# Performance work log

Measured on AMD Instinct MI355X. Metric: run time of the kernel, lower is better.

The kernel has to match this reference:

```python
import jax, jax.numpy as jnp
import numpy as np

N_NODES = 20000
N_EDGES = 320000
F_IN = 64
F = 64            # n_features
K = 32            # n_basis_funcs
R = 3             # n_refinements
R_MAX = 2.5       # radial basis span


def setup_inputs() -> dict:
    key = jax.random.key(0)
    ks = jax.random.split(key, 16)
    inp = {
        "x_dftb": jax.random.normal(ks[0], (N_NODES, 4, F_IN), jnp.float32),
        "coords": jax.random.normal(ks[1], (N_NODES, 3), jnp.float32),
        "dst_idx": jax.random.randint(ks[2], (N_EDGES,), 0, N_NODES, jnp.int32),
        "src_idx": jax.random.randint(ks[3], (N_EDGES,), 0, N_NODES, jnp.int32),
        # input TensorDense (degree-wise dense; bias only on the l=0 channel)
        "W_in0": jax.random.normal(ks[4], (F_IN, F), jnp.float32) / np.sqrt(F_IN),
        "W_in1": jax.random.normal(ks[5], (F_IN, F), jnp.float32) / np.sqrt(F_IN),
        "b_in": jnp.zeros((F,), jnp.float32),
        # per-refinement MessagePass params: basis projection (K->F) + scalar-channel bias
        "W_basis": jax.random.normal(ks[6], (R, K, F), jnp.float32) / np.sqrt(K),
        "b_basis": jnp.zeros((R, F), jnp.float32),
        # per-refinement CG path weights: 5 paths (0x0->0, 1.1->0, 0x1->1, 1x0->1, 1x1->1)
        "path_w": 0.05 * jax.random.normal(ks[7], (R, 5, F), jnp.float32),
        # output TensorDense (F -> 1)
        "W_out0": jax.random.normal(ks[8], (F, 1), jnp.float32) / np.sqrt(F),
        "W_out1": jax.random.normal(ks[9], (F, 1), jnp.float32) / np.sqrt(F),
        "b_out": jnp.zeros((1,), jnp.float32),
    }
    return inp


def _tensor_dense(x, W0, W1, b0):
    # degree-wise dense mixing of channels; bias only on l=0 (keeps equivariance)
    s = jnp.einsum('nf,fg->ng', x[:, 0], W0) + b0          # (N, G)
    v = jnp.einsum('nif,fg->nig', x[:, 1:4], W1)           # (N, 3, G)
    return jnp.concatenate([s[:, None], v], axis=1)        # (N, 4, G)


def reference(x_dftb, coords, dst_idx, src_idx,
              W_in0, W_in1, b_in, W_basis, b_basis, path_w,
              W_out0, W_out1, b_out):
    N = x_dftb.shape[0]
    # edge geometry: dist basis = gaussian radial x spherical harmonics (l<=1)
    r = coords[dst_idx] - coords[src_idx]                  # (E, 3)
    d = jnp.sqrt(jnp.sum(r * r, axis=-1) + 1e-12)          # (E,)
    rhat = r / d[:, None]
    sh = jnp.concatenate([jnp.ones_like(d)[:, None], rhat], axis=1)  # (E, 4)
    centers = jnp.linspace(0.0, R_MAX, K, dtype=jnp.float32)
    width = centers[1] - centers[0]
    rbf = jnp.exp(-((d[:, None] - centers) / width) ** 2)  # (E, K)
    basis = sh[:, :, None] * rbf[:, None, :]               # (E, 4, K)

    x = _tensor_dense(x_dftb, W_in0, W_in1, b_in)          # (N, 4, F)
    n_ref = W_basis.shape[0]
    for i in range(n_ref):
        # project basis channels K -> F, bias on scalar channel (use_basis_bias)
        g = jnp.einsum('elk,kf->elf', basis, W_basis[i])   # (E, 4, F)
        g = g.at[:, 0, :].add(b_basis[i])
        a = x[src_idx]                                     # gather src  (E, 4, F)
        a0, av = a[:, 0], a[:, 1:4]
        g0, gv = g[:, 0], g[:, 1:4]
        p = path_w[i]
        # CG-structured tensor product per feature channel
        m0 = p[0] * a0 * g0 + p[1] * jnp.sum(av * gv, axis=1)                 # (E, F)
        mv = (p[2][None, None] * a0[:, None] * gv
              + p[3][None, None] * av * g0[:, None]
              + p[4][None, None] * jnp.cross(av, gv, axis=1))                 # (E, 3, F)
        msg = jnp.concatenate([m0[:, None], mv], axis=1)                      # (E, 4, F)
        x = x + jax.ops.segment_sum(msg, dst_idx, num_segments=N)            # scatter-add
    return _tensor_dense(x, W_out0, W_out1, b_out)         # (N, 4, 1)
```

## Files before the change

### kernel.cpp

```cpp
#include <hip/hip_runtime.h>

#define N_NODES 20000
#define N_EDGES 320000
#define FF 64
#define KK 32
#define EPAD 460032
#define GT 64
#define BW 8

typedef _Float16 half4v __attribute__((ext_vector_type(4)));
typedef short bf16x8 __attribute__((ext_vector_type(8)));
typedef float fx4 __attribute__((ext_vector_type(4)));

__device__ __forceinline__ unsigned short f2bf(float x) {
    unsigned u = __float_as_uint(x);
    unsigned r = (u + 0x7FFFu + ((u >> 16) & 1u)) >> 16;
    return (unsigned short)r;
}

__global__ __launch_bounds__(256) void hist_k(const int* __restrict__ dst,
                                              int* __restrict__ cnt) {
    int e = blockIdx.x * 256 + threadIdx.x;
    if (e >= N_EDGES) return;
    atomicAdd(&cnt[dst[e]], 1);
}

__global__ __launch_bounds__(1024) void scan_k(const int* __restrict__ cnt,
                                               int* __restrict__ rps) {
    __shared__ int part[1024];
    int t = threadIdx.x;
    const int CH = 20;
    int lo = t * CH;
    int hi = lo + CH; if (hi > N_NODES) hi = N_NODES;
    int s = 0;
    for (int i = lo; i < hi && lo < N_NODES; ++i) s += (cnt[i] + 7) & ~7;
    if (lo >= N_NODES) s = 0;
    part[t] = s;
    __syncthreads();
    for (int off = 1; off < 1024; off <<= 1) {
        int tmp = (t >= off) ? part[t - off] : 0;
        __syncthreads();
        part[t] += tmp;
        __syncthreads();
    }
    int excl = part[t] - s;
    if (lo < N_NODES) {
        int run = excl;
        for (int i = lo; i < hi; ++i) { rps[i] = run; run += (cnt[i] + 7) & ~7; }
    }
    if (t == 1023) rps[N_NODES] = part[1023];
}

__global__ __launch_bounds__(256) void scatter_k(const float* __restrict__ coords,
                                                 const int* __restrict__ dst,
                                                 const int* __restrict__ src,
                                                 const int* __restrict__ rps,
                                                 int* __restrict__ fill,
                                                 int* __restrict__ esrcB,
                                                 float4* __restrict__ egeom) {
    int e = blockIdx.x * 256 + threadIdx.x;
    if (e >= N_EDGES) return;
    int di = dst[e], si = src[e];
    int pos = rps[di] + atomicAdd(&fill[di], 1);
    float rx = coords[di*3+0] - coords[si*3+0];
    float ry = coords[di*3+1] - coords[si*3+1];
    float rz = coords[di*3+2] - coords[si*3+2];
    float d = sqrtf(rx*rx + ry*ry + rz*rz + 1e-12f);
    float inv = 1.0f / d;
    esrcB[pos] = si * 512;
    egeom[pos] = make_float4(d, rx*inv, ry*inv, rz*inv);
}

__global__ __launch_bounds__(256) void pad_k(const int* __restrict__ rps,
                                             const int* __restrict__ cnt,
                                             int* __restrict__ esrcB,
                                             float4* __restrict__ egeom) {
    int n = blockIdx.x * 256 + threadIdx.x;
    if (n >= N_NODES) return;
    int fin = rps[n] + cnt[n];
    int stop = rps[n+1];
    for (int e = fin; e < stop; ++e) {
        esrcB[e] = N_NODES * 512;
        egeom[e] = make_float4(1.f, 0.f, 0.f, 0.f);
    }
}

template<int NR>
__global__ __launch_bounds__(256) void gmatM_k(const float4* __restrict__ egeom,
                                               const float* __restrict__ Wb,
                                               const int* __restrict__ rps,
                                               half4v* __restrict__ G4) {
    __shared__ __align__(16) short WtL[NR*KK*FF];
    __shared__ __align__(16) short rbfL[2][GT*40];
    int t = threadIdx.x;
    for (int idx = t; idx < NR*KK*FF; idx += 256)
        WtL[idx] = (short)f2bf(Wb[idx]);
    __syncthreads();

    int lane = t & 63, q = t >> 6;
    int kb = lane >> 4, cl = lane & 15;

    bf16x8 Bfr[NR][4];
    #pragma unroll
    for (int r = 0; r < NR; ++r) {
        #pragma unroll
        for (int nb = 0; nb < 4; ++nb) {
            bf16x8 fr;
            #pragma unroll
            for (int e2 = 0; e2 < 8; ++e2)
                fr[e2] = WtL[r*2048 + (kb*8 + e2)*64 + nb*16 + cl];
            Bfr[r][nb] = fr;
        }
    }

    int total = rps[N_NODES];
    int ntiles = (total + GT - 1) / GT;
    const float inv_w = 31.0f / 2.5f;
    int buf = 0;
    for (int tile = blockIdx.x; tile < ntiles; tile += gridDim.x) {
        int e0 = tile * GT;
        {
            int ew = t & 63;
            float d = egeom[e0 + ew].x;
            float t0 = d * inv_w;
            int k0 = (int)floorf(t0 + 0.5f) - 4;
            if (k0 < 0) k0 = 0;
            if (k0 > KK - 9) k0 = KK - 9;
            bf16x8 pk;
            #pragma unroll
            for (int i2 = 0; i2 < 8; ++i2) {
                int j = q*8 + i2;
                float dt = t0 - (float)j;
                float v = (j >= k0 && j < k0 + 9) ? __expf(-dt * dt) : 0.f;
                pk[i2] = (short)f2bf(v);
            }
            *(bf16x8*)(&rbfL[buf][ew*40 + q*8]) = pk;
        }
        __syncthreads();
        bf16x8 afr = *(const bf16x8*)(&rbfL[buf][(q*16 + cl)*40 + kb*8]);
        int eg = (e0 + q*16 + kb*4) >> 2;
        #pragma unroll
        for (int r = 0; r < NR; ++r) {
            #pragma unroll
            for (int nb = 0; nb < 4; ++nb) {
                fx4 dacc = {0.f, 0.f, 0.f, 0.f};
                dacc = __builtin_amdgcn_mfma_f32_16x16x32_bf16(afr, Bfr[r][nb],
                                                               dacc, 0, 0, 0);
                half4v hv;
                hv[0] = (_Float16)dacc[0]; hv[1] = (_Float16)dacc[1];
                hv[2] = (_Float16)dacc[2]; hv[3] = (_Float16)dacc[3];
                G4[(size_t)r*(EPAD/4)*64 + (size_t)eg*64 + nb*16 + cl] = hv;
            }
        }
        buf ^= 1;
    }
}

__global__ __launch_bounds__(256) void node_inM_k(const float* __restrict__ x_dftb,
                                                  const float* __restrict__ W0,
                                                  const float* __restrict__ W1,
                                                  const float* __restrict__ bin,
                                                  float* __restrict__ x,
                                                  half4v* __restrict__ xh) {
    int t = threadIdx.x;
    int q = t >> 6, lane = t & 63;
    int kb = lane >> 4, cl = lane & 15;
    int w = blockIdx.x * 4 + q;
    if (w >= N_NODES / 16) return;
    int n0 = w * 16;

    bf16x8 BF[2][4][2];
    #pragma unroll
    for (int cb = 0; cb < 4; ++cb) {
        #pragma unroll
        for (int kf = 0; kf < 2; ++kf) {
            bf16x8 f0, f1;
            #pragma unroll
            for (int j = 0; j < 8; ++j) {
                int k = kf*32 + kb*8 + j;
                f0[j] = (short)f2bf(W0[k*64 + cb*16 + cl]);
                f1[j] = (short)f2bf(W1[k*64 + cb*16 + cl]);
            }
            BF[0][cb][kf] = f0;
            BF[1][cb][kf] = f1;
        }
    }
    float bb[4];
    #pragma unroll
    for (int cb = 0; cb < 4; ++cb) bb[cb] = bin[cb*16 + cl];

    fx4 acc[4][4];
    #pragma unroll
    for (int l = 0; l < 4; ++l) {
        const float* xr = x_dftb + (size_t)(n0 + cl)*256 + l*64 + kb*8;
        float4 v0 = *(const float4*)(xr);
        float4 v1 = *(const float4*)(xr + 4);
        float4 v2 = *(const float4*)(xr + 32);
        float4 v3 = *(const float4*)(xr + 36);
        bf16x8 a0, a1;
        a0[0]=(short)f2bf(v0.x); a0[1]=(short)f2bf(v0.y);
        a0[2]=(short)f2bf(v0.z); a0[3]=(short)f2bf(v0.w);
        a0[4]=(short)f2bf(v1.x); a0[5]=(short)f2bf(v1.y);
        a0[6]=(short)f2bf(v1.z); a0[7]=(short)f2bf(v1.w);
        a1[0]=(short)f2bf(v2.x); a1[1]=(short)f2bf(v2.y);
        a1[2]=(short)f2bf(v2.z); a1[3]=(short)f2bf(v2.w);
        a1[4]=(short)f2bf(v3.x); a1[5]=(short)f2bf(v3.y);
        a1[6]=(short)f2bf(v3.z); a1[7]=(short)f2bf(v3.w);
        const int wsel = (l == 0) ? 0 : 1;
        #pragma unroll
        for (int cb = 0; cb < 4; ++cb) {
            fx4 c = {0.f, 0.f, 0.f, 0.f};
            c = __builtin_amdgcn_mfma_f32_16x16x32_bf16(a0, BF[wsel][cb][0], c, 0, 0, 0);
            c = __builtin_amdgcn_mfma_f32_16x16x32_bf16(a1, BF[wsel][cb][1], c, 0, 0, 0);
            acc[l][cb] = c;
        }
    }

    #pragma unroll
    for (int cb = 0; cb < 4; ++cb) {
        int f = cb*16 + cl;
        #pragma unroll
        for (int reg = 0; reg < 4; ++reg) {
            int n = n0 + kb*4 + reg;
            float a0v = acc[0][cb][reg] + bb[cb];
            float a1v = acc[1][cb][reg];
            float a2v = acc[2][cb][reg];
            float a3v = acc[3][cb][reg];
            *(float4*)(x + (size_t)n*256 + f*4) = make_float4(a0v, a1v, a2v, a3v);
            half4v hs;
            hs[0] = (_Float16)a0v; hs[1] = (_Float16)a1v;
            hs[2] = (_Float16)a2v; hs[3] = (_Float16)a3v;
            xh[(size_t)n*64 + f] = hs;
        }
    }
}

__global__ __launch_bounds__(256) void node_in_k(const float* __restrict__ x_dftb,
                                                 const float* __restrict__ W0,
                                                 const float* __restrict__ W1,
                                                 const float* __restrict__ bin,
                                                 float* __restrict__ x,
                                                 half4v* __restrict__ xh) {
    int t = threadIdx.x;
    int q = t >> 6, f = t & 63;
    int n = blockIdx.x * 4 + q;
    float w0r[64], w1r[64];
    #pragma unroll
    for (int k = 0; k < 64; ++k) { w0r[k] = W0[k*64 + f]; w1r[k] = W1[k*64 + f]; }
    float a0 = bin[f], a1 = 0.f, a2 = 0.f, a3 = 0.f;
    const float4* xr = (const float4*)(x_dftb + (size_t)n * 256);
    #pragma unroll
    for (int j = 0; j < 16; ++j) {
        float4 x0 = xr[j];
        float4 x1 = xr[16 + j];
        float4 x2 = xr[32 + j];
        float4 x3 = xr[48 + j];
        a0 += x0.x*w0r[4*j] + x0.y*w0r[4*j+1] + x0.z*w0r[4*j+2] + x0.w*w0r[4*j+3];
        a1 += x1.x*w1r[4*j] + x1.y*w1r[4*j+1] + x1.z*w1r[4*j+2] + x1.w*w1r[4*j+3];
        a2 += x2.x*w1r[4*j] + x2.y*w1r[4*j+1] + x2.z*w1r[4*j+2] + x2.w*w1r[4*j+3];
        a3 += x3.x*w1r[4*j] + x3.y*w1r[4*j+1] + x3.z*w1r[4*j+2] + x3.w*w1r[4*j+3];
    }
    *(float4*)(x + (size_t)n*256 + f*4) = make_float4(a0, a1, a2, a3);
    if (xh) {
        half4v hs;
        hs[0] = (_Float16)a0; hs[1] = (_Float16)a1;
        hs[2] = (_Float16)a2; hs[3] = (_Float16)a3;
        xh[(size_t)n*64 + f] = hs;
    }
}

template<int LAST>
__global__ __launch_bounds__(256) void msg_fast_k(const int* __restrict__ rps,
                                                  const int* __restrict__ esrcB,
                                                  const float4* __restrict__ egeom,
                                                  const half4v* __restrict__ G4,
                                                  const float* __restrict__ bbv,
                                                  const float* __restrict__ pw,
                                                  const float* __restrict__ xo_f,
                                                  const half4v* __restrict__ xo_h,
                                                  float* __restrict__ xn_f,
                                                  half4v* __restrict__ xn_h,
                                                  const float* __restrict__ Wo0,
                                                  const float* __restrict__ Wo1,
                                                  const float* __restrict__ bo,
                                                  float* __restrict__ out) {
    int t = threadIdx.x;
    int q = t >> 6, f = t & 63;

    float b_f = bbv[f];
    float p0 = pw[f], p1 = pw[64+f], p2 = pw[128+f], p3 = pw[192+f], p4 = pw[256+f];
    float w0 = 0.f, w1 = 0.f;
    if (LAST) { w0 = Wo0[f]; w1 = Wo1[f]; }

    const char* xob = (const char*)xo_h;
    int fb = f * 8;

    for (int n = blockIdx.x * 4 + q; n < N_NODES; n += gridDim.x * 4) {
        float4 self = *(const float4*)(xo_f + (size_t)n*256 + f*4);
        float acc0 = self.x, acc1 = self.y, acc2 = self.z, acc3 = self.w;

        int beg = rps[n], end = rps[n+1];
        for (int e0 = beg; e0 < end; e0 += BW) {
            int4 oa = *(const int4*)(esrcB + e0);
            int4 ob = *(const int4*)(esrcB + e0 + 4);
            int off[BW] = {oa.x, oa.y, oa.z, oa.w, ob.x, ob.y, ob.z, ob.w};
            half4v h[BW];
            #pragma unroll
            for (int j = 0; j < BW; ++j)
                h[j] = *(const half4v*)(xob + (size_t)(unsigned)off[j] + fb);
            half4v ga = G4[(size_t)(e0 >> 2)*64 + f];
            half4v gb = G4[(size_t)((e0 >> 2) + 1)*64 + f];
            float Gv[BW] = {(float)ga[0], (float)ga[1], (float)ga[2], (float)ga[3],
                            (float)gb[0], (float)gb[1], (float)gb[2], (float)gb[3]};
            float4 g4[BW];
            #pragma unroll
            for (int j = 0; j < BW; ++j) g4[j] = egeom[e0 + j];

            #pragma unroll
            for (int j = 0; j < BW; ++j) {
                float A0 = (float)h[j][0], A1 = (float)h[j][1];
                float A2 = (float)h[j][2], A3 = (float)h[j][3];
                float G = Gv[j];
                float ry = g4[j].y, rz = g4[j].z, rw_ = g4[j].w;
                float g0v = G + b_f;
                float dotav = A1*ry + A2*rz + A3*rw_;
                acc0 += p0*A0*g0v + p1*dotav*G;
                float tA = p2*A0*G, tB = p3*g0v, tC = p4*G;
                acc1 += tA*ry  + tB*A1 + tC*(A2*rw_ - A3*rz);
                acc2 += tA*rz  + tB*A2 + tC*(A3*ry  - A1*rw_);
                acc3 += tA*rw_ + tB*A3 + tC*(A1*rz  - A2*ry);
            }
        }

        if (LAST) {
            float s0 = acc0 * w0, s1 = acc1 * w1, s2 = acc2 * w1, s3 = acc3 * w1;
            #pragma unroll
            for (int off2 = 32; off2 >= 1; off2 >>= 1) {
                s0 += __shfl_down(s0, off2, 64);
                s1 += __shfl_down(s1, off2, 64);
                s2 += __shfl_down(s2, off2, 64);
                s3 += __shfl_down(s3, off2, 64);
            }
            if (f == 0) {
                float b = bo[0];
                out[n*4 + 0] = s0 + b;
                out[n*4 + 1] = s1;
                out[n*4 + 2] = s2;
                out[n*4 + 3] = s3;
            }
        } else {
            *(float4*)(xn_f + (size_t)n*256 + f*4) = make_float4(acc0, acc1, acc2, acc3);
            half4v hs;
            hs[0] = (_Float16)acc0; hs[1] = (_Float16)acc1;
            hs[2] = (_Float16)acc2; hs[3] = (_Float16)acc3;
            xn_h[(size_t)n*64 + f] = hs;
        }
    }
}

__global__ __launch_bounds__(256) void msg_slow_k(const int* __restrict__ rps,
                                                  const int* __restrict__ cnt,
                                                  const int* __restrict__ esrcB,
                                                  const float4* __restrict__ egeom,
                                                  const float* __restrict__ Wb,
                                                  const float* __restrict__ bbv,
                                                  const float* __restrict__ pw,
                                                  const float* __restrict__ xo_f,
                                                  float* __restrict__ xn_f) {
    int t = threadIdx.x;
    int n = blockIdx.x * 4 + (t >> 6);
    int f = t & 63;
    float wreg[KK];
    #pragma unroll
    for (int k = 0; k < KK; ++k) wreg[k] = Wb[k*64 + f];
    float4 self = *(const float4*)(xo_f + (size_t)n*256 + f*4);
    float acc0 = self.x, acc1 = self.y, acc2 = self.z, acc3 = self.w;
    float b_f = bbv[f];
    float p0 = pw[f], p1 = pw[64+f], p2 = pw[128+f], p3 = pw[192+f], p4 = pw[256+f];
    const float wdt = 2.5f / 31.0f, inv_w = 31.0f / 2.5f;
    float ck = wdt * (float)(f & 31);
    int beg = rps[n], end = beg + cnt[n];
    const char* xob = (const char*)xo_f;
    for (int e = beg; e < end; ++e) {
        int off = esrcB[e];
        float4 g4 = egeom[e];
        float4 v = *(const float4*)(xob + ((size_t)(unsigned)off << 1) + f*16);
        float tt = (g4.x - ck) * inv_w;
        float my_rbf = __expf(-tt * tt);
        float Gs = 0.f;
        #pragma unroll
        for (int k = 0; k < KK; ++k) Gs += __shfl(my_rbf, k, 64) * wreg[k];
        float g0v = Gs + b_f;
        float dotav = v.y*g4.y + v.z*g4.z + v.w*g4.w;
        acc0 += p0*v.x*g0v + p1*dotav*Gs;
        float tA = p2*v.x*Gs, tB = p3*g0v, tC = p4*Gs;
        acc1 += tA*g4.y + tB*v.y + tC*(v.z*g4.w - v.w*g4.z);
        acc2 += tA*g4.z + tB*v.z + tC*(v.w*g4.y - v.y*g4.w);
        acc3 += tA*g4.w + tB*v.w + tC*(v.y*g4.z - v.z*g4.y);
    }
    *(float4*)(xn_f + (size_t)n*256 + f*4) = make_float4(acc0, acc1, acc2, acc3);
}

__global__ __launch_bounds__(256) void node_out_k(const float* __restrict__ x,
                                                  const float* __restrict__ W0,
                                                  const float* __restrict__ W1,
                                                  const float* __restrict__ bout,
                                                  float* __restrict__ out) {
    int n = blockIdx.x * 4 + (threadIdx.x >> 6);
    int f = threadIdx.x & 63;
    float w0 = W0[f], w1 = W1[f];
    float4 v = *(const float4*)(x + (size_t)n*256 + f*4);
    float s0 = v.x * w0, s1 = v.y * w1, s2 = v.z * w1, s3 = v.w * w1;
    #pragma unroll
    for (int off = 32; off >= 1; off >>= 1) {
        s0 += __shfl_down(s0, off, 64);
        s1 += __shfl_down(s1, off, 64);
        s2 += __shfl_down(s2, off, 64);
        s3 += __shfl_down(s3, off, 64);
    }
    if (f == 0) {
        float b = bout[0];
        out[n*4 + 0] = s0 + b;
        out[n*4 + 1] = s1;
        out[n*4 + 2] = s2;
        out[n*4 + 3] = s3;
    }
}

extern "C" void kernel_launch(void* const* d_in, const int* in_sizes, int n_in,
                              void* d_out, int out_size, void* d_ws, size_t ws_size,
                              hipStream_t stream) {
    const float* x_dftb  = (const float*)d_in[0];
    const float* coords  = (const float*)d_in[1];
    const int*   dst     = (const int*)  d_in[2];
    const int*   src     = (const int*)  d_in[3];
    const float* W_in0   = (const float*)d_in[4];
    const float* W_in1   = (const float*)d_in[5];
    const float* b_in    = (const float*)d_in[6];
    const float* W_basis = (const float*)d_in[7];
    const float* b_basis = (const float*)d_in[8];
    const float* path_w  = (const float*)d_in[9];
    const float* W_out0  = (const float*)d_in[10];
    const float* W_out1  = (const float*)d_in[11];
    const float* b_out   = (const float*)d_in[12];
    float* out = (float*)d_out;

    const size_t XF = (size_t)N_NODES * 256 * 4;
    const size_t XH = (size_t)(N_NODES + 1) * 64 * 8;
    const size_t EG = (size_t)EPAD * 16;
    const size_t ES = (size_t)EPAD * 4;
    const size_t GP = (size_t)EPAD * 64 * 2;
    const size_t RP = (((size_t)(N_NODES + 1) * 4) + 15) & ~(size_t)15;
    const size_t CF = (size_t)N_NODES * 4;

    const size_t base_need = 2*XF + 2*XH + EG + ES + RP + 2*CF;
    int planes = (ws_size >= base_need + 3*GP) ? 3
               : (ws_size >= base_need + 1*GP) ? 1 : 0;

    char* p = (char*)d_ws;
    float*   xA = (float*)p;  p += XF;
    float*   xB = (float*)p;  p += XF;
    half4v*  hA = nullptr; half4v* hB = nullptr;
    half4v*  Gm = nullptr;
    if (planes) {
        hA = (half4v*)p;  p += XH;
        hB = (half4v*)p;  p += XH;
        Gm = (half4v*)p;  p += (size_t)planes * GP;
    }
    float4* egeom = (float4*)p;  p += EG;
    int*    esrcB = (int*)p;     p += ES;
    int*    rps   = (int*)p;     p += RP;
    int*    cnt   = (int*)p;     p += CF;
    int*    fill  = (int*)p;     p += CF;

    hipMemsetAsync(cnt,  0, CF, stream);
    hipMemsetAsync(fill, 0, CF, stream);
    if (planes) {
        hipMemsetAsync((char*)hA + (size_t)N_NODES*512, 0, 512, stream);
        hipMemsetAsync((char*)hB + (size_t)N_NODES*512, 0, 512, stream);
    }

    hist_k   <<<(N_EDGES+255)/256, 256, 0, stream>>>(dst, cnt);
    scan_k   <<<1, 1024, 0, stream>>>(cnt, rps);
    scatter_k<<<(N_EDGES+255)/256, 256, 0, stream>>>(coords, dst, src, rps, fill,
                                                     esrcB, egeom);
    pad_k    <<<(N_NODES+255)/256, 256, 0, stream>>>(rps, cnt, esrcB, egeom);
    if (planes)
        node_inM_k<<<(N_NODES/16 + 3)/4, 256, 0, stream>>>(x_dftb, W_in0, W_in1,
                                                           b_in, xA, hA);
    else
        node_in_k<<<N_NODES/4, 256, 0, stream>>>(x_dftb, W_in0, W_in1, b_in, xA,
                                                 nullptr);
    if (planes == 3)
        gmatM_k<3><<<1536, 256, 0, stream>>>(egeom, W_basis, rps, Gm);

    float*  xo = xA; float*  xn = xB;
    half4v* ho = hA; half4v* hn = hB;
    for (int i = 0; i < 3; ++i) {
        if (planes) {
            if (planes == 1)
                gmatM_k<1><<<1536, 256, 0, stream>>>(egeom, W_basis + i*KK*FF, rps, Gm);
            const half4v* Gp = Gm + ((planes == 3) ? (size_t)i*(EPAD/4)*64 : 0);
            if (i < 2)
                msg_fast_k<0><<<2048, 256, 0, stream>>>(rps, esrcB, egeom, Gp,
                                                        b_basis + i*FF, path_w + i*5*FF,
                                                        xo, ho, xn, hn,
                                                        nullptr, nullptr, nullptr, nullptr);
            else
                msg_fast_k<1><<<2048, 256, 0, stream>>>(rps, esrcB, egeom, Gp,
                                                        b_basis + i*FF, path_w + i*5*FF,
                                                        xo, ho, nullptr, nullptr,
                                                        W_out0, W_out1, b_out, out);
        } else {
            msg_slow_k<<<N_NODES/4, 256, 0, stream>>>(rps, cnt, esrcB, egeom,
                                                      W_basis + i*KK*FF,
                                                      b_basis + i*FF, path_w + i*5*FF,
                                                      xo, xn);
        }
        float*  tf = xo; xo = xn; xn = tf;
        half4v* th = ho; ho = hn; hn = th;
    }
    if (!planes)
        node_out_k<<<N_NODES/4, 256, 0, stream>>>(xo, W_out0, W_out1, b_out, out);
}
```

Before: 271.0 us.

## Use packed fp16 math in message kernel with fp16 geometry planes

Adds a kernel that converts the per-edge direction vectors into packed fp16 planes grouped in blocks of 8 edges. The message kernel then does its per-edge tensor-product math in packed half2 arithmetic, two edges per instruction, and accumulates into fp32 once per 8-edge block. The launch also changes from a grid-stride loop over 2048 blocks to one node per wavefront with N/4 blocks. The aim is to halve ALU work and cut geometry bandwidth, at the cost of fp16 rounding inside each 8-edge partial sum.

Result: faster. 232.7 us (-14.1%).

```diff
diff --git a/kernel.cpp b/kernel.cpp
--- a/kernel.cpp
+++ b/kernel.cpp
@@ -9,6 +9,7 @@
 #define BW 8
 
 typedef _Float16 half4v __attribute__((ext_vector_type(4)));
+typedef _Float16 h2 __attribute__((ext_vector_type(2)));
 typedef short bf16x8 __attribute__((ext_vector_type(8)));
 typedef float fx4 __attribute__((ext_vector_type(4)));
 
@@ -16,6 +17,12 @@
     unsigned u = __float_as_uint(x);
     unsigned r = (u + 0x7FFFu + ((u >> 16) & 1u)) >> 16;
     return (unsigned short)r;
+}
+__device__ __forceinline__ h2 u2h(unsigned u) {
+    union { unsigned u; h2 h; } c; c.u = u; return c.h;
+}
+__device__ __forceinline__ unsigned h2u(h2 h) {
+    union { h2 h; unsigned u; } c; c.h = h; return c.u;
 }
 
 __global__ __launch_bounds__(256) void hist_k(const int* __restrict__ dst,
@@ -82,6 +89,27 @@
     for (int e = fin; e < stop; ++e) {
         esrcB[e] = N_NODES * 512;
         egeom[e] = make_float4(1.f, 0.f, 0.f, 0.f);
+    }
+}
+
+__global__ __launch_bounds__(256) void geomh_k(const float4* __restrict__ egeom,
+                                               const int* __restrict__ rps,
+                                               unsigned* __restrict__ gH) {
+    int b = blockIdx.x * 256 + threadIdx.x;
+    int total = rps[N_NODES];
+    if (b * 8 >= total) return;
+    float4 g[8];
+    #pragma unroll
+    for (int j = 0; j < 8; ++j) g[j] = egeom[b*8 + j];
+    unsigned* o = gH + (size_t)b * 12;
+    #pragma unroll
+    for (int p = 0; p < 4; ++p) {
+        h2 y; y[0] = (_Float16)g[2*p].y; y[1] = (_Float16)g[2*p+1].y;
+        h2 z; z[0] = (_Float16)g[2*p].z; z[1] = (_Float16)g[2*p+1].z;
+        h2 w; w[0] = (_Float16)g[2*p].w; w[1] = (_Float16)g[2*p+1].w;
+        o[0*4 + p] = h2u(y);
+        o[1*4 + p] = h2u(z);
+        o[2*4 + p] = h2u(w);
     }
 }
 
@@ -270,91 +298,115 @@
 }
 
 template<int LAST>
-__global__ __launch_bounds__(256) void msg_fast_k(const int* __restrict__ rps,
-                                                  const int* __restrict__ esrcB,
-                                                  const float4* __restrict__ egeom,
-                                                  const half4v* __restrict__ G4,
-                                                  const float* __restrict__ bbv,
-                                                  const float* __restrict__ pw,
-                                                  const float* __restrict__ xo_f,
-                                                  const half4v* __restrict__ xo_h,
-                                                  float* __restrict__ xn_f,
-                                                  half4v* __restrict__ xn_h,
-                                                  const float* __restrict__ Wo0,
-                                                  const float* __restrict__ Wo1,
-                                                  const float* __restrict__ bo,
-                                                  float* __restrict__ out) {
+__global__ __launch_bounds__(256) void msg_pk_k(const int* __restrict__ rps,
+                                                const int* __restrict__ esrcB,
+                                                const unsigned* __restrict__ gH,
+                                                const half4v* __restrict__ G4,
+                                                const float* __restrict__ bbv,
+                                                const float* __restrict__ pw,
+                                                const float* __restrict__ xo_f,
+                                                const half4v* __restrict__ xo_h,
+                                                float* __restrict__ xn_f,
+                                                half4v* __restrict__ xn_h,
+                                                const float* __restrict__ Wo0,
+                                                const float* __restrict__ Wo1,
+                                                const float* __restrict__ bo,
+                                                float* __restrict__ out) {
     int t = threadIdx.x;
     int q = t >> 6, f = t & 63;
+    int n = blockIdx.x * 4 + q;
+
+    float4 self = *(const float4*)(xo_f + (size_t)n*256 + f*4);
+    float acc0 = self.x, acc1 = self.y, acc2 = self.z, acc3 = self.w;
 
     float b_f = bbv[f];
-    float p0 = pw[f], p1 = pw[64+f], p2 = pw[128+f], p3 = pw[192+f], p4 = pw[256+f];
-    float w0 = 0.f, w1 = 0.f;
-    if (LAST) { w0 = Wo0[f]; w1 = Wo1[f]; }
+    _Float16 bh = (_Float16)b_f;
+    _Float16 p0h = (_Float16)pw[f],      p1h = (_Float16)pw[64+f];
+    _Float16 p2h = (_Float16)pw[128+f],  p3h = (_Float16)pw[192+f];
+    _Float16 p4h = (_Float16)pw[256+f];
+    h2 pb;  pb[0]=bh;  pb[1]=bh;
+    h2 pp0; pp0[0]=p0h; pp0[1]=p0h;
+    h2 pp1; pp1[0]=p1h; pp1[1]=p1h;
+    h2 pp2; pp2[0]=p2h; pp2[1]=p2h;
+    h2 pp3; pp3[0]=p3h; pp3[1]=p3h;
+    h2 pp4; pp4[0]=p4h; pp4[1]=p4h;
 
     const char* xob = (const char*)xo_h;
     int fb = f * 8;
-
-    for (int n = blockIdx.x * 4 + q; n < N_NODES; n += gridDim.x * 4) {
-        float4 self = *(const float4*)(xo_f + (size_t)n*256 + f*4);
-        float acc0 = self.x, acc1 = self.y, acc2 = self.z, acc3 = self.w;
-
-        int beg = rps[n], end = rps[n+1];
-        for (int e0 = beg; e0 < end; e0 += BW) {
-            int4 oa = *(const int4*)(esrcB + e0);
-            int4 ob = *(const int4*)(esrcB + e0 + 4);
-            int off[BW] = {oa.x, oa.y, oa.z, oa.w, ob.x, ob.y, ob.z, ob.w};
-            half4v h[BW];
-            #pragma unroll
-            for (int j = 0; j < BW; ++j)
-                h[j] = *(const half4v*)(xob + (size_t)(unsigned)off[j] + fb);
-            half4v ga = G4[(size_t)(e0 >> 2)*64 + f];
-            half4v gb = G4[(size_t)((e0 >> 2) + 1)*64 + f];
-            float Gv[BW] = {(float)ga[0], (float)ga[1], (float)ga[2], (float)ga[3],
-                            (float)gb[0], (float)gb[1], (float)gb[2], (float)gb[3]};
-            float4 g4[BW];
-            #pragma unroll
-            for (int j = 0; j < BW; ++j) g4[j] = egeom[e0 + j];
-
-            #pragma unroll
-            for (int j = 0; j < BW; ++j) {
-                float A0 = (float)h[j][0], A1 = (float)h[j][1];
-                float A2 = (float)h[j][2], A3 = (float)h[j][3];
-                float G = Gv[j];
-                float ry = g4[j].y, rz = g4[j].z, rw_ = g4[j].w;
-                float g0v = G + b_f;
-                float dotav = A1*ry + A2*rz + A3*rw_;
-                acc0 += p0*A0*g0v + p1*dotav*G;
-                float tA = p2*A0*G, tB = p3*g0v, tC = p4*G;
-                acc1 += tA*ry  + tB*A1 + tC*(A2*rw_ - A3*rz);
-                acc2 += tA*rz  + tB*A2 + tC*(A3*ry  - A1*rw_);
-                acc3 += tA*rw_ + tB*A3 + tC*(A1*rz  - A2*ry);
-            }
-        }
-
-        if (LAST) {
-            float s0 = acc0 * w0, s1 = acc1 * w1, s2 = acc2 * w1, s3 = acc3 * w1;
-            #pragma unroll
-            for (int off2 = 32; off2 >= 1; off2 >>= 1) {
-                s0 += __shfl_down(s0, off2, 64);
-                s1 += __shfl_down(s1, off2, 64);
-                s2 += __shfl_down(s2, off2, 64);
-                s3 += __shfl_down(s3, off2, 64);
-            }
-            if (f == 0) {
-                float b = bo[0];
-                out[n*4 + 0] = s0 + b;
-                out[n*4 + 1] = s1;
-                out[n*4 + 2] = s2;
-                out[n*4 + 3] = s3;
-            }
-        } else {
-            *(float4*)(xn_f + (size_t)n*256 + f*4) = make_float4(acc0, acc1, acc2, acc3);
-            half4v hs;
-            hs[0] = (_Float16)acc0; hs[1] = (_Float16)acc1;
-            hs[2] = (_Float16)acc2; hs[3] = (_Float16)acc3;
-            xn_h[(size_t)n*64 + f] = hs;
-        }
+    int beg = rps[n], end = rps[n+1];
+
+    for (int e0 = beg; e0 < end; e0 += BW) {
+        int4 oa = *(const int4*)(esrcB + e0);
+        int4 ob = *(const int4*)(esrcB + e0 + 4);
+        int off[BW] = {oa.x, oa.y, oa.z, oa.w, ob.x, ob.y, ob.z, ob.w};
+        half4v h[BW];
+        #pragma unroll
+        for (int j = 0; j < BW; ++j)
+            h[j] = *(const half4v*)(xob + (size_t)(unsigned)off[j] + fb);
+        uint2 gau = *(const uint2*)(G4 + (size_t)(e0 >> 2)*64 + f);
+        uint2 gbu = *(const uint2*)(G4 + (size_t)((e0 >> 2) + 1)*64 + f);
+        unsigned gpk[4] = {gau.x, gau.y, gbu.x, gbu.y};
+        const unsigned* gb_ = gH + (size_t)(e0 >> 3) * 12;
+        uint4 gyv = *(const uint4*)(gb_);
+        uint4 gzv = *(const uint4*)(gb_ + 4);
+        uint4 gwv = *(const uint4*)(gb_ + 8);
+        unsigned gyu[4] = {gyv.x, gyv.y, gyv.z, gyv.w};
+        unsigned gzu[4] = {gzv.x, gzv.y, gzv.z, gzv.w};
+        unsigned gwu[4] = {gwv.x, gwv.y, gwv.z, gwv.w};
+
+        h2 s0, s1, s2, s3;
+        s0[0]=(_Float16)0; s0[1]=(_Float16)0; s1 = s0; s2 = s0; s3 = s0;
+
+        #pragma unroll
+        for (int i = 0; i < 4; ++i) {
+            h2 a0; a0[0] = h[2*i][0]; a0[1] = h[2*i+1][0];
+            h2 a1; a1[0] = h[2*i][1]; a1[1] = h[2*i+1][1];
+            h2 a2; a2[0] = h[2*i][2]; a2[1] = h[2*i+1][2];
+            h2 a3; a3[0] = h[2*i][3]; a3[1] = h[2*i+1][3];
+            h2 G  = u2h(gpk[i]);
+            h2 ry = u2h(gyu[i]);
+            h2 rz = u2h(gzu[i]);
+            h2 rw = u2h(gwu[i]);
+
+            h2 g0v = G + pb;
+            h2 dot = a1*ry + a2*rz + a3*rw;
+            s0 += pp0*a0*g0v + pp1*dot*G;
+            h2 tA = pp2*a0*G;
+            h2 tB = pp3*g0v;
+            h2 tC = pp4*G;
+            s1 += tA*ry + tB*a1 + tC*(a2*rw - a3*rz);
+            s2 += tA*rz + tB*a2 + tC*(a3*ry - a1*rw);
+            s3 += tA*rw + tB*a3 + tC*(a1*rz - a2*ry);
+        }
+        acc0 += (float)s0[0] + (float)s0[1];
+        acc1 += (float)s1[0] + (float)s1[1];
+        acc2 += (float)s2[0] + (float)s2[1];
+        acc3 += (float)s3[0] + (float)s3[1];
+    }
+
+    if (LAST) {
+        float w0 = Wo0[f], w1 = Wo1[f];
+        float s0 = acc0 * w0, s1 = acc1 * w1, s2 = acc2 * w1, s3 = acc3 * w1;
+        #pragma unroll
+        for (int off2 = 32; off2 >= 1; off2 >>= 1) {
+            s0 += __shfl_down(s0, off2, 64);
+            s1 += __shfl_down(s1, off2, 64);
+            s2 += __shfl_down(s2, off2, 64);
+            s3 += __shfl_down(s3, off2, 64);
+        }
+        if (f == 0) {
+            float b = bo[0];
+            out[n*4 + 0] = s0 + b;
+            out[n*4 + 1] = s1;
+            out[n*4 + 2] = s2;
+            out[n*4 + 3] = s3;
+        }
+    } else {
+        *(float4*)(xn_f + (size_t)n*256 + f*4) = make_float4(acc0, acc1, acc2, acc3);
+        half4v hs;
+        hs[0] = (_Float16)acc0; hs[1] = (_Float16)acc1;
+        hs[2] = (_Float16)acc2; hs[3] = (_Float16)acc3;
+        xn_h[(size_t)n*64 + f] = hs;
     }
 }
 
@@ -450,10 +502,11 @@
     const size_t EG = (size_t)EPAD * 16;
     const size_t ES = (size_t)EPAD * 4;
     const size_t GP = (size_t)EPAD * 64 * 2;
+    const size_t GH = (size_t)(EPAD/8) * 48;
     const size_t RP = (((size_t)(N_NODES + 1) * 4) + 15) & ~(size_t)15;
     const size_t CF = (size_t)N_NODES * 4;
 
-    const size_t base_need = 2*XF + 2*XH + EG + ES + RP + 2*CF;
+    const size_t base_need = 2*XF + 2*XH + EG + ES + GH + RP + 2*CF;
     int planes = (ws_size >= base_need + 3*GP) ? 3
                : (ws_size >= base_need + 1*GP) ? 1 : 0;
 
@@ -462,10 +515,12 @@
     float*   xB = (float*)p;  p += XF;
     half4v*  hA = nullptr; half4v* hB = nullptr;
     half4v*  Gm = nullptr;
+    unsigned* gH = nullptr;
     if (planes) {
         hA = (half4v*)p;  p += XH;
         hB = (half4v*)p;  p += XH;
         Gm = (half4v*)p;  p += (size_t)planes * GP;
+        gH = (unsigned*)p; p += GH;
     }
     float4* egeom = (float4*)p;  p += EG;
     int*    esrcB = (int*)p;     p += ES;
@@ -485,12 +540,14 @@
     scatter_k<<<(N_EDGES+255)/256, 256, 0, stream>>>(coords, dst, src, rps, fill,
                                                      esrcB, egeom);
     pad_k    <<<(N_NODES+255)/256, 256, 0, stream>>>(rps, cnt, esrcB, egeom);
-    if (planes)
+    if (planes) {
+        geomh_k<<<(EPAD/8 + 255)/256, 256, 0, stream>>>(egeom, rps, gH);
         node_inM_k<<<(N_NODES/16 + 3)/4, 256, 0, stream>>>(x_dftb, W_in0, W_in1,
                                                            b_in, xA, hA);
-    else
+    } else {
         node_in_k<<<N_NODES/4, 256, 0, stream>>>(x_dftb, W_in0, W_in1, b_in, xA,
                                                  nullptr);
+    }
     if (planes == 3)
         gmatM_k<3><<<1536, 256, 0, stream>>>(egeom, W_basis, rps, Gm);
 
@@ -502,15 +559,15 @@
                 gmatM_k<1><<<1536, 256, 0, stream>>>(egeom, W_basis + i*KK*FF, rps, Gm);
             const half4v* Gp = Gm + ((planes == 3) ? (size_t)i*(EPAD/4)*64 : 0);
             if (i < 2)
-                msg_fast_k<0><<<2048, 256, 0, stream>>>(rps, esrcB, egeom, Gp,
-                                                        b_basis + i*FF, path_w + i*5*FF,
-                                                        xo, ho, xn, hn,
-                                                        nullptr, nullptr, nullptr, nullptr);
+                msg_pk_k<0><<<N_NODES/4, 256, 0, stream>>>(rps, esrcB, gH, Gp,
+                                                           b_basis + i*FF, path_w + i*5*FF,
+                                                           xo, ho, xn, hn,
+                                                           nullptr, nullptr, nullptr, nullptr);
             else
-                msg_fast_k<1><<<2048, 256, 0, stream>>>(rps, esrcB, egeom, Gp,
-                                                        b_basis + i*FF, path_w + i*5*FF,
-                                                        xo, ho, nullptr, nullptr,
-                                                        W_out0, W_out1, b_out, out);
+                msg_pk_k<1><<<N_NODES/4, 256, 0, stream>>>(rps, esrcB, gH, Gp,
+                                                           b_basis + i*FF, path_w + i*5*FF,
+                                                           xo, ho, nullptr, nullptr,
+                                                           W_out0, W_out1, b_out, out);
         } else {
             msg_slow_k<<<N_NODES/4, 256, 0, stream>>>(rps, cnt, esrcB, egeom,
                                                       W_basis + i*KK*FF,
```
